# Optimization experiments

Hardware: AMD Instinct MI355X
Metric: run time of the kernel (lower is better)

The kernel has to match this reference:

```python
import jax, jax.numpy as jnp
import numpy as np

S, B, I, O, H, E, K = 128, 32, 512, 512, 512, 8, 2


def setup_inputs() -> dict:
    key = jax.random.key(0)
    ks = jax.random.split(key, 6)
    s = 0.02
    return {
        "x": jax.random.normal(ks[0], (S, B, I), dtype=jnp.float32),
        "router_w": jax.random.normal(ks[1], (I, E), dtype=jnp.float32) * s,
        "router_b": jnp.zeros((E,), dtype=jnp.float32),
        # per-expert LSTM controller params (proxy for DNC_Adapted recurrent expert)
        "Wi": jax.random.normal(ks[2], (E, I, 4 * H), dtype=jnp.float32) * s,
        "Wh": jax.random.normal(ks[3], (E, H, 4 * H), dtype=jnp.float32) * s,
        "b": jnp.zeros((E, 4 * H), dtype=jnp.float32),
        "Wo": jax.random.normal(ks[4], (E, H, O), dtype=jnp.float32) * s,
        "bo": jnp.zeros((E, O), dtype=jnp.float32),
    }


def _expert(x_seq, Wi, Wh, b, Wo, bo):
    # x_seq: [S, B, I] (dense, zero-padded at non-routed positions, as in the
    # original per-expert dispatch); single-layer LSTM controller + output proj.
    Bsz = x_seq.shape[1]
    Hd = Wh.shape[0]

    def step(carry, xt):
        h, c = carry
        gates = xt @ Wi + h @ Wh + b            # [B, 4H]
        i_, f_, g_, o_ = jnp.split(gates, 4, axis=-1)
        c = jax.nn.sigmoid(f_) * c + jax.nn.sigmoid(i_) * jnp.tanh(g_)
        h = jax.nn.sigmoid(o_) * jnp.tanh(c)
        return (h, c), h @ Wo + bo              # [B, O]

    init = (jnp.zeros((Bsz, Hd), x_seq.dtype), jnp.zeros((Bsz, Hd), x_seq.dtype))
    _, ys = jax.lax.scan(step, init, x_seq)
    return ys                                   # [S, B, O]


def reference(x, router_w, router_b, Wi, Wh, b, Wo, bo):
    S_, B_, I_ = x.shape
    N = S_ * B_
    flat_x = x.reshape(N, I_)
    logits = flat_x @ router_w + router_b        # [N, E]
    top_vals, top_idx = jax.lax.top_k(logits, K) # [N, K]
    rw = jax.nn.softmax(top_vals, axis=1)        # routing weights over top-k

    # mask[k, e, n] = 1 if token n routed to expert e at rank k
    mask = (top_idx.T[:, None, :] == jnp.arange(E)[None, :, None]).astype(x.dtype)
    # dense zero-padded per-(k, expert) inputs, matching the original dispatch
    expert_x = (mask[..., None] * flat_x[None, None]).reshape(K, E, S_, B_, I_)

    run_e = jax.vmap(_expert, in_axes=(0, 0, 0, 0, 0, 0))            # over experts
    run_ke = jax.vmap(run_e, in_axes=(0, None, None, None, None, None))  # over k
    out = run_ke(expert_x, Wi, Wh, b, Wo, bo)    # [K, E, S, B, O]
    out = out.reshape(K, E, N, -1)

    # scatter-add weighted expert outputs back to token positions
    y = jnp.einsum('ken,nk,keno->no', mask, rw, out)
    return y.reshape(S_, B_, -1)
```

## Files before the change

### kernel.cpp

```cpp
#include <hip/hip_runtime.h>
#include <hip/hip_bf16.h>
#include <cstdint>
#include <cstddef>

#define DI __device__ __forceinline__

typedef __bf16 bf16_t;
typedef bf16_t bf16x8 __attribute__((ext_vector_type(8)));
typedef float f32x4 __attribute__((ext_vector_type(4)));
typedef unsigned int u32;
typedef unsigned long long u64;

constexpr int S_ = 128, B_ = 32, I_ = 512, H_ = 512, O_ = 512, E_ = 8;
constexpr int Ntok = S_ * B_;
constexpr int G4 = 4 * H_;
constexpr int ROWS = 64;
constexpr int SLOT = E_ * ROWS * H_;

constexpr size_t OFF_CNT  = 0;
constexpr size_t OFF_BAR  = 64;
constexpr size_t OFF_XCDM = 640;
constexpr size_t OFF_XCDG = 1216;
constexpr size_t OFF_MASK = 2048;
constexpr size_t OFF_HALL = 16384;
constexpr size_t SLOT_B   = (size_t)SLOT * 2;
constexpr size_t ZERO_BYTES = OFF_HALL + SLOT_B;
constexpr size_t OFF_TIDX = OFF_HALL + 129ull * SLOT_B;
constexpr size_t OFF_RW   = OFF_TIDX + (size_t)Ntok * 2 * 4;
constexpr size_t OFF_LIST = OFF_RW + (size_t)Ntok * 2 * 4;
constexpr size_t OFF_WHT  = OFF_LIST + (size_t)E_ * Ntok * 4;
constexpr size_t OFF_WIT  = OFF_WHT + (size_t)E_ * G4 * H_ * 2;
constexpr size_t OFF_WOT  = OFF_WIT + (size_t)E_ * G4 * I_ * 2;
constexpr size_t OFF_XP   = OFF_WOT + (size_t)E_ * O_ * H_ * 2;
constexpr size_t WS_NEED  = OFF_XP + (size_t)Ntok * 2 * G4 * 2;

DI float sigf(float v) { return 1.f / (1.f + __expf(-v)); }
DI float tanh_(float v) { float e = __expf(2.f * v); return 1.f - 2.f / (e + 1.f); }

DI bf16x8 pack8(float4 a, float4 b) {
  bf16x8 r;
  r[0] = (bf16_t)a.x; r[1] = (bf16_t)a.y; r[2] = (bf16_t)a.z; r[3] = (bf16_t)a.w;
  r[4] = (bf16_t)b.x; r[5] = (bf16_t)b.y; r[6] = (bf16_t)b.z; r[7] = (bf16_t)b.w;
  return r;
}

__global__ void k_prep(const float* __restrict__ src, bf16_t* __restrict__ dst,
                       int Cdim, int perm) {
  __shared__ float tile[32][33];
  int ct = blockIdx.x, kt = blockIdx.y, e = blockIdx.z;
  const float* se = src + (size_t)e * 512 * Cdim;
  bf16_t* de = dst + (size_t)e * Cdim * 512;
  int c = threadIdx.x & 31, r0 = threadIdx.x >> 5;
  for (int s = 0; s < 4; s++) {
    int rr = r0 + s * 8;
    tile[rr][c] = se[(size_t)(kt * 32 + rr) * Cdim + ct * 32 + c];
  }
  __syncthreads();
  int kk = threadIdx.x & 31, c0 = threadIdx.x >> 5;
  for (int s = 0; s < 4; s++) {
    int cc = c0 + s * 8;
    int cg = ct * 32 + cc;
    int vc = perm ? (((cg & 511) >> 4) * 64 + (cg >> 9) * 16 + (cg & 15)) : cg;
    int kg = kt * 32 + kk;
    de[(size_t)vc * 512 + (kg ^ ((vc & 7) << 3))] = (bf16_t)tile[kk][cc];
  }
}

__global__ void k_router(const float* __restrict__ x, const float* __restrict__ rww,
                         const float* __restrict__ rwb, int* __restrict__ topidx,
                         float* __restrict__ rwgt, int* __restrict__ lists,
                         int* __restrict__ cnt, u64* __restrict__ rowmask) {
  int n = blockIdx.x * 4 + (threadIdx.x >> 6);
  int l = threadIdx.x & 63;
  const float* xr = x + (size_t)n * I_;
  double acc[8] = {0, 0, 0, 0, 0, 0, 0, 0};
  for (int ii = 0; ii < 8; ii++) {
    int i = l * 8 + ii;
    double xv = (double)xr[i];
    const float* wr = rww + i * 8;
#pragma unroll
    for (int e = 0; e < 8; e++) acc[e] += xv * (double)wr[e];
  }
#pragma unroll
  for (int off = 32; off > 0; off >>= 1)
#pragma unroll
    for (int e = 0; e < 8; e++) acc[e] += __shfl_xor(acc[e], off, 64);
  if (l == 0) {
    double lg[8];
    for (int e = 0; e < 8; e++) lg[e] = acc[e] + (double)rwb[e];
    int e0 = 0;
    for (int e = 1; e < 8; e++) if (lg[e] > lg[e0]) e0 = e;
    int e1 = -1;
    for (int e = 0; e < 8; e++) { if (e == e0) continue; if (e1 < 0 || lg[e] > lg[e1]) e1 = e; }
    double ed = exp(lg[e1] - lg[e0]);
    float p0 = (float)(1.0 / (1.0 + ed));
    float p1 = (float)(ed / (1.0 + ed));
    topidx[n * 2] = e0; topidx[n * 2 + 1] = e1;
    rwgt[n * 2] = p0; rwgt[n * 2 + 1] = p1;
    int t = n >> 5, bi = n & 31;
    int p = atomicAdd(&cnt[e0], 1); lists[e0 * Ntok + p] = n * 2;
    p = atomicAdd(&cnt[e1], 1);     lists[e1 * Ntok + p] = n * 2 + 1;
    atomicOr(&rowmask[e0 * 128 + t], 1ull << bi);
    atomicOr(&rowmask[e1 * 128 + t], 1ull << (32 + bi));
  }
}

DI void gemm64(const bf16_t* Als, const bf16_t* Bls, int wv, int l, f32x4* acc) {
  int ar = l & 15, kg = l >> 4;
  int arow = wv * 16 + ar;
  int aswz = (ar & 7) << 3;
#pragma unroll
  for (int ks = 0; ks < 16; ks++) {
    int kb = ks * 32 + kg * 8;
    bf16x8 a = *(const bf16x8*)&Als[arow * 512 + (kb ^ aswz)];
#pragma unroll
    for (int q = 0; q < 4; q++) {
      bf16x8 b = *(const bf16x8*)&Bls[(q * 16 + ar) * 512 + (kb ^ aswz)];
      acc[q] = __builtin_amdgcn_mfma_f32_16x16x32_bf16(a, b, acc[q], 0, 0, 0);
    }
  }
}

__launch_bounds__(256, 1)
__global__ void k_xp(const float* __restrict__ x, const bf16_t* __restrict__ Wit,
                     const int* __restrict__ lists, const int* __restrict__ cnt,
                     bf16_t* __restrict__ xp) {
  __shared__ bf16_t Als[64 * 512];
  __shared__ bf16_t Bls[64 * 512];
  __shared__ int ents[64];
  int e = blockIdx.z, ct = blockIdx.x, rt = blockIdx.y;
  int count = cnt[e];
  int rbase = rt * 64;
  if (rbase >= count) return;
  int tid = threadIdx.x;
  if (tid < 64) ents[tid] = (rbase + tid < count) ? lists[e * Ntok + rbase + tid] : -1;
  __syncthreads();
  int rr = tid >> 2, qq = tid & 3;
  int ent = ents[rr];
  int swzr = (rr & 7) << 3;
  if (ent >= 0) {
    const float* xr = x + (size_t)(ent >> 1) * I_ + qq * 128;
#pragma unroll
    for (int i2 = 0; i2 < 16; i2++) {
      float4 a = *(const float4*)(xr + i2 * 8);
      float4 b = *(const float4*)(xr + i2 * 8 + 4);
      *(bf16x8*)&Als[rr * 512 + ((qq * 128 + i2 * 8) ^ swzr)] = pack8(a, b);
    }
  } else {
    bf16x8 z;
    for (int j = 0; j < 8; j++) z[j] = (bf16_t)0.f;
#pragma unroll
    for (int i2 = 0; i2 < 16; i2++)
      *(bf16x8*)&Als[rr * 512 + ((qq * 128 + i2 * 8) ^ swzr)] = z;
  }
  const bf16_t* bs = Wit + ((size_t)e * G4 + ct * 64) * 512;
#pragma unroll
  for (int i2 = 0; i2 < 16; i2++) {
    int o = (i2 * 256 + tid) * 8;
    *(bf16x8*)&Bls[o] = *(const bf16x8*)&bs[o];
  }
  __syncthreads();
  f32x4 acc[4];
  for (int q = 0; q < 4; q++) { f32x4 z = {0.f, 0.f, 0.f, 0.f}; acc[q] = z; }
  int l = tid & 63, wv = tid >> 6;
  gemm64(Als, Bls, wv, l, acc);
#pragma unroll
  for (int q = 0; q < 4; q++)
#pragma unroll
    for (int r = 0; r < 4; r++) {
      int rr2 = wv * 16 + ((l >> 4) << 2) + r;
      int ent2 = ents[rr2];
      if (ent2 >= 0)
        xp[(size_t)ent2 * G4 + ct * 64 + q * 16 + (l & 15)] = (bf16_t)acc[q][r];
    }
}

DI void gbar(u32* bar_e, int idx, bool fence) {
  if (fence) __threadfence();
  __syncthreads();
  if (threadIdx.x == 0) {
    __hip_atomic_fetch_add(bar_e, 1u, __ATOMIC_RELAXED, __HIP_MEMORY_SCOPE_AGENT);
    u32 target = 32u * (u32)(idx + 1);
    while (__hip_atomic_load(bar_e, __ATOMIC_RELAXED, __HIP_MEMORY_SCOPE_AGENT) < target)
      __builtin_amdgcn_s_sleep(2);
  }
  __syncthreads();
  if (fence) __threadfence();
}

__launch_bounds__(256, 1)
__global__ void k_rec(const bf16_t* __restrict__ Wht, const bf16_t* __restrict__ xp,
                      const float* __restrict__ bgate, bf16_t* __restrict__ hall,
                      const u64* __restrict__ rowmask, u32* __restrict__ bar,
                      u32* __restrict__ xcdm, u32* __restrict__ xcdg) {
  __shared__ bf16_t Bls[64 * 512];
  int bid = blockIdx.x;
  int e = bid & 7, w = bid >> 3;
  int tid = threadIdx.x, l = tid & 63, wv = tid >> 6;
  const bf16_t* bs = Wht + ((size_t)e * G4 + w * 64) * 512;
#pragma unroll
  for (int i2 = 0; i2 < 16; i2++) {
    int o = (i2 * 256 + tid) * 8;
    *(bf16x8*)&Bls[o] = *(const bf16x8*)&bs[o];
  }
  int jl = l & 15, j = w * 16 + jl;
  float bq[4];
#pragma unroll
  for (int q = 0; q < 4; q++) bq[q] = bgate[e * G4 + q * 512 + j];
  int xcd = __builtin_amdgcn_s_getreg(20 | (3 << 11)) & 15;
  if (tid == 0) {
    __hip_atomic_fetch_or(&xcdm[e * 16], 1u << xcd, __ATOMIC_RELAXED, __HIP_MEMORY_SCOPE_AGENT);
    __hip_atomic_fetch_or(xcdg, 1u << xcd, __ATOMIC_RELAXED, __HIP_MEMORY_SCOPE_AGENT);
  }
  u32* mybar = &bar[e * 16];
  gbar(mybar, 0, true);
  u32 me = __hip_atomic_load(&xcdm[e * 16], __ATOMIC_RELAXED, __HIP_MEMORY_SCOPE_AGENT);
  u32 mg = __hip_atomic_load(xcdg, __ATOMIC_RELAXED, __HIP_MEMORY_SCOPE_AGENT);
  bool fast = (__popc(me) == 1) && (__popc(mg) > 1);
  float creg[4] = {0.f, 0.f, 0.f, 0.f};
  int ar = l & 15, kg = l >> 4;
  int arow = wv * 16 + ar;
  int aswz = (ar & 7) << 3;
  for (int t = 0; t < 128; t++) {
    const bf16_t* hc = hall + (size_t)t * SLOT + e * ROWS * 512;
    bf16x8 af[16];
#pragma unroll
    for (int ks = 0; ks < 16; ks++)
      af[ks] = *(const bf16x8*)&hc[arow * 512 + ks * 32 + kg * 8];
    f32x4 acc[4];
    for (int q = 0; q < 4; q++) { f32x4 z = {0.f, 0.f, 0.f, 0.f}; acc[q] = z; }
#pragma unroll
    for (int ks = 0; ks < 16; ks++) {
      int kb = ks * 32 + kg * 8;
#pragma unroll
      for (int q = 0; q < 4; q++) {
        bf16x8 b = *(const bf16x8*)&Bls[(q * 16 + ar) * 512 + (kb ^ aswz)];
        acc[q] = __builtin_amdgcn_mfma_f32_16x16x32_bf16(af[ks], b, acc[q], 0, 0, 0);
      }
    }
    u64 mask = rowmask[e * 128 + t];
    bf16_t* hn = hall + (size_t)(t + 1) * SLOT + e * ROWS * 512;
#pragma unroll
    for (int r = 0; r < 4; r++) {
      int row = wv * 16 + ((l >> 4) << 2) + r;
      float gi = acc[0][r] + bq[0];
      float gf = acc[1][r] + bq[1];
      float gg = acc[2][r] + bq[2];
      float go = acc[3][r] + bq[3];
      if ((mask >> row) & 1ull) {
        int n2 = ((t << 5) + (row & 31)) * 2 + (row >> 5);
        const bf16_t* xr = xp + (size_t)n2 * G4;
        gi += (float)xr[j];        gf += (float)xr[512 + j];
        gg += (float)xr[1024 + j]; go += (float)xr[1536 + j];
      }
      float cn = sigf(gf) * creg[r] + sigf(gi) * tanh_(gg);
      creg[r] = cn;
      float hv = sigf(go) * tanh_(cn);
      hn[row * 512 + j] = (bf16_t)hv;
    }
    if (t < 127) gbar(mybar, t + 1, !fast);
  }
}

__launch_bounds__(256, 1)
__global__ void k_out(const bf16_t* __restrict__ hall, const bf16_t* __restrict__ Wot,
                      const float* __restrict__ bo, const int* __restrict__ lists,
                      const int* __restrict__ cnt, const float* __restrict__ rwgt,
                      float* __restrict__ y) {
  __shared__ bf16_t Als[64 * 512];
  __shared__ bf16_t Bls[64 * 512];
  __shared__ int ents[64];
  __shared__ float rws[64];
  int e = blockIdx.z, ct = blockIdx.x, rt = blockIdx.y;
  int count = cnt[e];
  if (rt * 64 >= count) return;
  int tid = threadIdx.x;
  if (tid < 64) {
    int ent = (rt * 64 + tid < count) ? lists[e * Ntok + rt * 64 + tid] : -1;
    ents[tid] = ent;
    rws[tid] = (ent >= 0) ? rwgt[ent] : 0.f;
  }
  __syncthreads();
  int rr = tid >> 2, qq = tid & 3;
  int ent = ents[rr];
  int swzr = (rr & 7) << 3;
  if (ent >= 0) {
    int n = ent >> 1, kk = ent & 1, t = n >> 5;
    const bf16_t* hr = hall + (size_t)(t + 1) * SLOT +
                       (size_t)(e * ROWS + kk * 32 + (n & 31)) * 512 + qq * 128;
#pragma unroll
    for (int i2 = 0; i2 < 16; i2++) {
      bf16x8 v = *(const bf16x8*)(hr + i2 * 8);
      *(bf16x8*)&Als[rr * 512 + ((qq * 128 + i2 * 8) ^ swzr)] = v;
    }
  } else {
    bf16x8 z;
    for (int jz = 0; jz < 8; jz++) z[jz] = (bf16_t)0.f;
#pragma unroll
    for (int i2 = 0; i2 < 16; i2++)
      *(bf16x8*)&Als[rr * 512 + ((qq * 128 + i2 * 8) ^ swzr)] = z;
  }
  const bf16_t* bsrc = Wot + ((size_t)e * O_ + ct * 64) * 512;
#pragma unroll
  for (int i2 = 0; i2 < 16; i2++) {
    int o = (i2 * 256 + tid) * 8;
    *(bf16x8*)&Bls[o] = *(const bf16x8*)&bsrc[o];
  }
  __syncthreads();
  f32x4 acc[4];
  for (int q = 0; q < 4; q++) { f32x4 z = {0.f, 0.f, 0.f, 0.f}; acc[q] = z; }
  int l = tid & 63, wv = tid >> 6;
  gemm64(Als, Bls, wv, l, acc);
  float boq[4];
#pragma unroll
  for (int q = 0; q < 4; q++) boq[q] = bo[e * O_ + ct * 64 + q * 16 + (l & 15)];
#pragma unroll
  for (int q = 0; q < 4; q++)
#pragma unroll
    for (int r = 0; r < 4; r++) {
      int rr2 = wv * 16 + ((l >> 4) << 2) + r;
      int ent2 = ents[rr2];
      if (ent2 >= 0) {
        float val = (acc[q][r] + boq[q]) * rws[rr2];
        unsafeAtomicAdd(&y[(size_t)(ent2 >> 1) * O_ + ct * 64 + q * 16 + (l & 15)], val);
      }
    }
}

extern "C" void kernel_launch(void* const* d_in, const int* in_sizes, int n_in,
                              void* d_out, int out_size, void* d_ws, size_t ws_size,
                              hipStream_t stream) {
  (void)in_sizes; (void)n_in;
  const float* x   = (const float*)d_in[0];
  const float* rww = (const float*)d_in[1];
  const float* rwb = (const float*)d_in[2];
  const float* Wi  = (const float*)d_in[3];
  const float* Wh  = (const float*)d_in[4];
  const float* bg  = (const float*)d_in[5];
  const float* Wo  = (const float*)d_in[6];
  const float* bo  = (const float*)d_in[7];
  float* y = (float*)d_out;
  char* ws = (char*)d_ws;

  if (ws_size < WS_NEED) {
    hipMemsetAsync(d_out, 0, (size_t)out_size * 4, stream);
    return;
  }

  int* cnt     = (int*)(ws + OFF_CNT);
  u32* bar     = (u32*)(ws + OFF_BAR);
  u32* xcdm    = (u32*)(ws + OFF_XCDM);
  u32* xcdg    = (u32*)(ws + OFF_XCDG);
  u64* rowmask = (u64*)(ws + OFF_MASK);
  bf16_t* hall = (bf16_t*)(ws + OFF_HALL);
  int* topidx  = (int*)(ws + OFF_TIDX);
  float* rwgt  = (float*)(ws + OFF_RW);
  int* lists   = (int*)(ws + OFF_LIST);
  bf16_t* Wht  = (bf16_t*)(ws + OFF_WHT);
  bf16_t* Wit  = (bf16_t*)(ws + OFF_WIT);
  bf16_t* Wot  = (bf16_t*)(ws + OFF_WOT);
  bf16_t* xp   = (bf16_t*)(ws + OFF_XP);

  hipMemsetAsync(ws, 0, ZERO_BYTES, stream);
  hipMemsetAsync(d_out, 0, (size_t)out_size * 4, stream);

  k_prep<<<dim3(G4 / 32, 16, 8), 256, 0, stream>>>(Wi, Wit, G4, 0);
  k_prep<<<dim3(G4 / 32, 16, 8), 256, 0, stream>>>(Wh, Wht, G4, 1);
  k_prep<<<dim3(O_ / 32, 16, 8), 256, 0, stream>>>(Wo, Wot, O_, 0);
  k_router<<<Ntok / 4, 256, 0, stream>>>(x, rww, rwb, topidx, rwgt, lists, cnt, rowmask);
  k_xp<<<dim3(32, 64, 8), 256, 0, stream>>>(x, Wit, lists, cnt, xp);
  k_rec<<<256, 256, 0, stream>>>(Wht, xp, bg, hall, rowmask, bar, xcdm, xcdg);
  k_out<<<dim3(8, 64, 8), 256, 0, stream>>>(hall, Wot, bo, lists, cnt, rwgt, y);
}
```

Baseline: 1.212 ms.

## Replace counter barrier with per-block flag sync, prefetch interleaved xp, persist tiles

The per-expert atomic-counter barrier in the recurrent kernel becomes per-block step flags that each wave polls across all 32 peer blocks with a wave-wide vote. The xp gate pre-activations are stored gate-interleaved so each row needs one 8-byte load, and that load for step t+1 is issued before the step-t MFMA work. The k_xp and k_out grids shrink to 16 row-tiles that loop over row chunks, so each block loads its weight tile into shared memory once. This aims to cut barrier latency and the exposed global loads on the serial recurrence path, at the cost of more polling traffic.

```diff
diff --git a/kernel.cpp b/kernel.cpp
--- a/kernel.cpp
+++ b/kernel.cpp
@@ -18,10 +18,11 @@
 constexpr int SLOT = E_ * ROWS * H_;
 
 constexpr size_t OFF_CNT  = 0;
-constexpr size_t OFF_BAR  = 64;
-constexpr size_t OFF_XCDM = 640;
-constexpr size_t OFF_XCDG = 1216;
+constexpr size_t OFF_XCDM = 64;
+constexpr size_t OFF_XCDG = 704;
+constexpr size_t OFF_DFL  = 1024;
 constexpr size_t OFF_MASK = 2048;
+constexpr size_t OFF_FLG  = 10240;
 constexpr size_t OFF_HALL = 16384;
 constexpr size_t SLOT_B   = (size_t)SLOT * 2;
 constexpr size_t ZERO_BYTES = OFF_HALL + SLOT_B;
@@ -36,6 +37,7 @@
 
 DI float sigf(float v) { return 1.f / (1.f + __expf(-v)); }
 DI float tanh_(float v) { float e = __expf(2.f * v); return 1.f - 2.f / (e + 1.f); }
+DI float bfu(u32 s) { u32 x = (s & 0xffffu) << 16; return __builtin_bit_cast(float, x); }
 
 DI bf16x8 pack8(float4 a, float4 b) {
   bf16x8 r;
@@ -124,75 +126,66 @@
 __launch_bounds__(256, 1)
 __global__ void k_xp(const float* __restrict__ x, const bf16_t* __restrict__ Wit,
                      const int* __restrict__ lists, const int* __restrict__ cnt,
-                     bf16_t* __restrict__ xp) {
+                     bf16_t* __restrict__ xp2) {
   __shared__ bf16_t Als[64 * 512];
   __shared__ bf16_t Bls[64 * 512];
   __shared__ int ents[64];
-  int e = blockIdx.z, ct = blockIdx.x, rt = blockIdx.y;
+  int e = blockIdx.z, ct = blockIdx.x, rt0 = blockIdx.y;
   int count = cnt[e];
-  int rbase = rt * 64;
-  if (rbase >= count) return;
   int tid = threadIdx.x;
-  if (tid < 64) ents[tid] = (rbase + tid < count) ? lists[e * Ntok + rbase + tid] : -1;
-  __syncthreads();
-  int rr = tid >> 2, qq = tid & 3;
-  int ent = ents[rr];
-  int swzr = (rr & 7) << 3;
-  if (ent >= 0) {
-    const float* xr = x + (size_t)(ent >> 1) * I_ + qq * 128;
-#pragma unroll
-    for (int i2 = 0; i2 < 16; i2++) {
-      float4 a = *(const float4*)(xr + i2 * 8);
-      float4 b = *(const float4*)(xr + i2 * 8 + 4);
-      *(bf16x8*)&Als[rr * 512 + ((qq * 128 + i2 * 8) ^ swzr)] = pack8(a, b);
-    }
-  } else {
-    bf16x8 z;
-    for (int j = 0; j < 8; j++) z[j] = (bf16_t)0.f;
-#pragma unroll
-    for (int i2 = 0; i2 < 16; i2++)
-      *(bf16x8*)&Als[rr * 512 + ((qq * 128 + i2 * 8) ^ swzr)] = z;
-  }
   const bf16_t* bs = Wit + ((size_t)e * G4 + ct * 64) * 512;
 #pragma unroll
   for (int i2 = 0; i2 < 16; i2++) {
     int o = (i2 * 256 + tid) * 8;
     *(bf16x8*)&Bls[o] = *(const bf16x8*)&bs[o];
   }
-  __syncthreads();
-  f32x4 acc[4];
-  for (int q = 0; q < 4; q++) { f32x4 z = {0.f, 0.f, 0.f, 0.f}; acc[q] = z; }
   int l = tid & 63, wv = tid >> 6;
-  gemm64(Als, Bls, wv, l, acc);
-#pragma unroll
-  for (int q = 0; q < 4; q++)
-#pragma unroll
-    for (int r = 0; r < 4; r++) {
-      int rr2 = wv * 16 + ((l >> 4) << 2) + r;
-      int ent2 = ents[rr2];
-      if (ent2 >= 0)
-        xp[(size_t)ent2 * G4 + ct * 64 + q * 16 + (l & 15)] = (bf16_t)acc[q][r];
-    }
-}
-
-DI void gbar(u32* bar_e, int idx, bool fence) {
-  if (fence) __threadfence();
-  __syncthreads();
-  if (threadIdx.x == 0) {
-    __hip_atomic_fetch_add(bar_e, 1u, __ATOMIC_RELAXED, __HIP_MEMORY_SCOPE_AGENT);
-    u32 target = 32u * (u32)(idx + 1);
-    while (__hip_atomic_load(bar_e, __ATOMIC_RELAXED, __HIP_MEMORY_SCOPE_AGENT) < target)
-      __builtin_amdgcn_s_sleep(2);
-  }
-  __syncthreads();
-  if (fence) __threadfence();
+  int rr = tid >> 2, qq = tid & 3;
+  int swzr = (rr & 7) << 3;
+  for (int rbase = rt0 * 64; rbase < count; rbase += 16 * 64) {
+    __syncthreads();
+    if (tid < 64) ents[tid] = (rbase + tid < count) ? lists[e * Ntok + rbase + tid] : -1;
+    __syncthreads();
+    int ent = ents[rr];
+    if (ent >= 0) {
+      const float* xr = x + (size_t)(ent >> 1) * I_ + qq * 128;
+#pragma unroll
+      for (int i2 = 0; i2 < 16; i2++) {
+        float4 a = *(const float4*)(xr + i2 * 8);
+        float4 b = *(const float4*)(xr + i2 * 8 + 4);
+        *(bf16x8*)&Als[rr * 512 + ((qq * 128 + i2 * 8) ^ swzr)] = pack8(a, b);
+      }
+    } else {
+      bf16x8 z;
+      for (int jz = 0; jz < 8; jz++) z[jz] = (bf16_t)0.f;
+#pragma unroll
+      for (int i2 = 0; i2 < 16; i2++)
+        *(bf16x8*)&Als[rr * 512 + ((qq * 128 + i2 * 8) ^ swzr)] = z;
+    }
+    __syncthreads();
+    f32x4 acc[4];
+    for (int q = 0; q < 4; q++) { f32x4 z = {0.f, 0.f, 0.f, 0.f}; acc[q] = z; }
+    gemm64(Als, Bls, wv, l, acc);
+#pragma unroll
+    for (int q = 0; q < 4; q++)
+#pragma unroll
+      for (int r = 0; r < 4; r++) {
+        int rr2 = wv * 16 + ((l >> 4) << 2) + r;
+        int ent2 = ents[rr2];
+        if (ent2 >= 0) {
+          int g = ct * 64 + q * 16 + (l & 15);
+          xp2[(size_t)ent2 * G4 + (size_t)(g & 511) * 4 + (g >> 9)] = (bf16_t)acc[q][r];
+        }
+      }
+  }
 }
 
 __launch_bounds__(256, 1)
-__global__ void k_rec(const bf16_t* __restrict__ Wht, const bf16_t* __restrict__ xp,
+__global__ void k_rec(const bf16_t* __restrict__ Wht, const bf16_t* __restrict__ xp2,
                       const float* __restrict__ bgate, bf16_t* __restrict__ hall,
-                      const u64* __restrict__ rowmask, u32* __restrict__ bar,
-                      u32* __restrict__ xcdm, u32* __restrict__ xcdg) {
+                      const u64* __restrict__ rowmask, u32* __restrict__ flags,
+                      u32* __restrict__ dfl, u32* __restrict__ xcdm,
+                      u32* __restrict__ xcdg) {
   __shared__ bf16_t Bls[64 * 512];
   int bid = blockIdx.x;
   int e = bid & 7, w = bid >> 3;
@@ -211,22 +204,59 @@
   if (tid == 0) {
     __hip_atomic_fetch_or(&xcdm[e * 16], 1u << xcd, __ATOMIC_RELAXED, __HIP_MEMORY_SCOPE_AGENT);
     __hip_atomic_fetch_or(xcdg, 1u << xcd, __ATOMIC_RELAXED, __HIP_MEMORY_SCOPE_AGENT);
-  }
-  u32* mybar = &bar[e * 16];
-  gbar(mybar, 0, true);
+    __hip_atomic_store(&dfl[e * 32 + w], 1u, __ATOMIC_RELEASE, __HIP_MEMORY_SCOPE_AGENT);
+  }
+  for (;;) {
+    u32 f = __hip_atomic_load(&dfl[e * 32 + (l & 31)], __ATOMIC_RELAXED, __HIP_MEMORY_SCOPE_AGENT);
+    if (__all((int)(f >= 1u))) break;
+    __builtin_amdgcn_s_sleep(1);
+  }
+  __builtin_amdgcn_sched_barrier(0);
   u32 me = __hip_atomic_load(&xcdm[e * 16], __ATOMIC_RELAXED, __HIP_MEMORY_SCOPE_AGENT);
   u32 mg = __hip_atomic_load(xcdg, __ATOMIC_RELAXED, __HIP_MEMORY_SCOPE_AGENT);
   bool fast = (__popc(me) == 1) && (__popc(mg) > 1);
+  __syncthreads();
+
   float creg[4] = {0.f, 0.f, 0.f, 0.f};
   int ar = l & 15, kg = l >> 4;
   int arow = wv * 16 + ar;
   int aswz = (ar & 7) << 3;
+  int r0 = wv * 16 + (kg << 2);
+  const ushort* xpu = (const ushort*)xp2;
+
+  uint2 xpc[4], xpn[4];
+  {
+    u64 mk = rowmask[e * 128];
+#pragma unroll
+    for (int r = 0; r < 4; r++) {
+      int row = r0 + r;
+      xpc[r].x = 0; xpc[r].y = 0;
+      if ((mk >> row) & 1ull) {
+        int n2 = ((row & 31)) * 2 + (row >> 5);
+        xpc[r] = *(const uint2*)(xpu + ((size_t)n2 * G4 + j * 4));
+      }
+    }
+  }
+
   for (int t = 0; t < 128; t++) {
     const bf16_t* hc = hall + (size_t)t * SLOT + e * ROWS * 512;
     bf16x8 af[16];
 #pragma unroll
     for (int ks = 0; ks < 16; ks++)
       af[ks] = *(const bf16x8*)&hc[arow * 512 + ks * 32 + kg * 8];
+#pragma unroll
+    for (int r = 0; r < 4; r++) { xpn[r].x = 0; xpn[r].y = 0; }
+    if (t < 127) {
+      u64 mk = rowmask[e * 128 + t + 1];
+#pragma unroll
+      for (int r = 0; r < 4; r++) {
+        int row = r0 + r;
+        if ((mk >> row) & 1ull) {
+          int n2 = (((t + 1) << 5) + (row & 31)) * 2 + (row >> 5);
+          xpn[r] = *(const uint2*)(xpu + ((size_t)n2 * G4 + j * 4));
+        }
+      }
+    }
     f32x4 acc[4];
     for (int q = 0; q < 4; q++) { f32x4 z = {0.f, 0.f, 0.f, 0.f}; acc[q] = z; }
 #pragma unroll
@@ -238,27 +268,36 @@
         acc[q] = __builtin_amdgcn_mfma_f32_16x16x32_bf16(af[ks], b, acc[q], 0, 0, 0);
       }
     }
-    u64 mask = rowmask[e * 128 + t];
     bf16_t* hn = hall + (size_t)(t + 1) * SLOT + e * ROWS * 512;
 #pragma unroll
     for (int r = 0; r < 4; r++) {
-      int row = wv * 16 + ((l >> 4) << 2) + r;
-      float gi = acc[0][r] + bq[0];
-      float gf = acc[1][r] + bq[1];
-      float gg = acc[2][r] + bq[2];
-      float go = acc[3][r] + bq[3];
-      if ((mask >> row) & 1ull) {
-        int n2 = ((t << 5) + (row & 31)) * 2 + (row >> 5);
-        const bf16_t* xr = xp + (size_t)n2 * G4;
-        gi += (float)xr[j];        gf += (float)xr[512 + j];
-        gg += (float)xr[1024 + j]; go += (float)xr[1536 + j];
-      }
+      int row = r0 + r;
+      float gi = acc[0][r] + bq[0] + bfu(xpc[r].x);
+      float gf = acc[1][r] + bq[1] + bfu(xpc[r].x >> 16);
+      float gg = acc[2][r] + bq[2] + bfu(xpc[r].y);
+      float go = acc[3][r] + bq[3] + bfu(xpc[r].y >> 16);
       float cn = sigf(gf) * creg[r] + sigf(gi) * tanh_(gg);
       creg[r] = cn;
-      float hv = sigf(go) * tanh_(cn);
-      hn[row * 512 + j] = (bf16_t)hv;
-    }
-    if (t < 127) gbar(mybar, t + 1, !fast);
+      hn[row * 512 + j] = (bf16_t)(sigf(go) * tanh_(cn));
+    }
+#pragma unroll
+    for (int r = 0; r < 4; r++) xpc[r] = xpn[r];
+    if (t < 127) {
+      __syncthreads();
+      if (!fast) __threadfence();
+      if (tid == 0)
+        __hip_atomic_store(&flags[e * 64 + w], (u32)(t + 1), __ATOMIC_RELAXED,
+                           __HIP_MEMORY_SCOPE_AGENT);
+      u32 tgt = (u32)(t + 1);
+      for (;;) {
+        u32 f = __hip_atomic_load(&flags[e * 64 + (l & 31)], __ATOMIC_RELAXED,
+                                  __HIP_MEMORY_SCOPE_AGENT);
+        if (__all((int)(f >= tgt))) break;
+        __builtin_amdgcn_s_sleep(1);
+      }
+      __builtin_amdgcn_sched_barrier(0);
+      if (!fast) __threadfence();
+    }
   }
 }
 
@@ -271,60 +310,62 @@
   __shared__ bf16_t Bls[64 * 512];
   __shared__ int ents[64];
   __shared__ float rws[64];
-  int e = blockIdx.z, ct = blockIdx.x, rt = blockIdx.y;
+  int e = blockIdx.z, ct = blockIdx.x, rt0 = blockIdx.y;
   int count = cnt[e];
-  if (rt * 64 >= count) return;
   int tid = threadIdx.x;
-  if (tid < 64) {
-    int ent = (rt * 64 + tid < count) ? lists[e * Ntok + rt * 64 + tid] : -1;
-    ents[tid] = ent;
-    rws[tid] = (ent >= 0) ? rwgt[ent] : 0.f;
-  }
-  __syncthreads();
-  int rr = tid >> 2, qq = tid & 3;
-  int ent = ents[rr];
-  int swzr = (rr & 7) << 3;
-  if (ent >= 0) {
-    int n = ent >> 1, kk = ent & 1, t = n >> 5;
-    const bf16_t* hr = hall + (size_t)(t + 1) * SLOT +
-                       (size_t)(e * ROWS + kk * 32 + (n & 31)) * 512 + qq * 128;
-#pragma unroll
-    for (int i2 = 0; i2 < 16; i2++) {
-      bf16x8 v = *(const bf16x8*)(hr + i2 * 8);
-      *(bf16x8*)&Als[rr * 512 + ((qq * 128 + i2 * 8) ^ swzr)] = v;
-    }
-  } else {
-    bf16x8 z;
-    for (int jz = 0; jz < 8; jz++) z[jz] = (bf16_t)0.f;
-#pragma unroll
-    for (int i2 = 0; i2 < 16; i2++)
-      *(bf16x8*)&Als[rr * 512 + ((qq * 128 + i2 * 8) ^ swzr)] = z;
-  }
   const bf16_t* bsrc = Wot + ((size_t)e * O_ + ct * 64) * 512;
 #pragma unroll
   for (int i2 = 0; i2 < 16; i2++) {
     int o = (i2 * 256 + tid) * 8;
     *(bf16x8*)&Bls[o] = *(const bf16x8*)&bsrc[o];
   }
-  __syncthreads();
-  f32x4 acc[4];
-  for (int q = 0; q < 4; q++) { f32x4 z = {0.f, 0.f, 0.f, 0.f}; acc[q] = z; }
   int l = tid & 63, wv = tid >> 6;
-  gemm64(Als, Bls, wv, l, acc);
+  int rr = tid >> 2, qq = tid & 3;
+  int swzr = (rr & 7) << 3;
   float boq[4];
 #pragma unroll
   for (int q = 0; q < 4; q++) boq[q] = bo[e * O_ + ct * 64 + q * 16 + (l & 15)];
-#pragma unroll
-  for (int q = 0; q < 4; q++)
-#pragma unroll
-    for (int r = 0; r < 4; r++) {
-      int rr2 = wv * 16 + ((l >> 4) << 2) + r;
-      int ent2 = ents[rr2];
-      if (ent2 >= 0) {
-        float val = (acc[q][r] + boq[q]) * rws[rr2];
-        unsafeAtomicAdd(&y[(size_t)(ent2 >> 1) * O_ + ct * 64 + q * 16 + (l & 15)], val);
-      }
-    }
+  for (int rbase = rt0 * 64; rbase < count; rbase += 16 * 64) {
+    __syncthreads();
+    if (tid < 64) {
+      int ent = (rbase + tid < count) ? lists[e * Ntok + rbase + tid] : -1;
+      ents[tid] = ent;
+      rws[tid] = (ent >= 0) ? rwgt[ent] : 0.f;
+    }
+    __syncthreads();
+    int ent = ents[rr];
+    if (ent >= 0) {
+      int n = ent >> 1, kk = ent & 1, t = n >> 5;
+      const bf16_t* hr = hall + (size_t)(t + 1) * SLOT +
+                         (size_t)(e * ROWS + kk * 32 + (n & 31)) * 512 + qq * 128;
+#pragma unroll
+      for (int i2 = 0; i2 < 16; i2++) {
+        bf16x8 v = *(const bf16x8*)(hr + i2 * 8);
+        *(bf16x8*)&Als[rr * 512 + ((qq * 128 + i2 * 8) ^ swzr)] = v;
+      }
+    } else {
+      bf16x8 z;
+      for (int jz = 0; jz < 8; jz++) z[jz] = (bf16_t)0.f;
+#pragma unroll
+      for (int i2 = 0; i2 < 16; i2++)
+        *(bf16x8*)&Als[rr * 512 + ((qq * 128 + i2 * 8) ^ swzr)] = z;
+    }
+    __syncthreads();
+    f32x4 acc[4];
+    for (int q = 0; q < 4; q++) { f32x4 z = {0.f, 0.f, 0.f, 0.f}; acc[q] = z; }
+    gemm64(Als, Bls, wv, l, acc);
+#pragma unroll
+    for (int q = 0; q < 4; q++)
+#pragma unroll
+      for (int r = 0; r < 4; r++) {
+        int rr2 = wv * 16 + ((l >> 4) << 2) + r;
+        int ent2 = ents[rr2];
+        if (ent2 >= 0) {
+          float val = (acc[q][r] + boq[q]) * rws[rr2];
+          unsafeAtomicAdd(&y[(size_t)(ent2 >> 1) * O_ + ct * 64 + q * 16 + (l & 15)], val);
+        }
+      }
+  }
 }
 
 extern "C" void kernel_launch(void* const* d_in, const int* in_sizes, int n_in,
@@ -348,10 +389,11 @@
   }
 
   int* cnt     = (int*)(ws + OFF_CNT);
-  u32* bar     = (u32*)(ws + OFF_BAR);
   u32* xcdm    = (u32*)(ws + OFF_XCDM);
   u32* xcdg    = (u32*)(ws + OFF_XCDG);
+  u32* dfl     = (u32*)(ws + OFF_DFL);
   u64* rowmask = (u64*)(ws + OFF_MASK);
+  u32* flags   = (u32*)(ws + OFF_FLG);
   bf16_t* hall = (bf16_t*)(ws + OFF_HALL);
   int* topidx  = (int*)(ws + OFF_TIDX);
   float* rwgt  = (float*)(ws + OFF_RW);
@@ -359,7 +401,7 @@
   bf16_t* Wht  = (bf16_t*)(ws + OFF_WHT);
   bf16_t* Wit  = (bf16_t*)(ws + OFF_WIT);
   bf16_t* Wot  = (bf16_t*)(ws + OFF_WOT);
-  bf16_t* xp   = (bf16_t*)(ws + OFF_XP);
+  bf16_t* xp2  = (bf16_t*)(ws + OFF_XP);
 
   hipMemsetAsync(ws, 0, ZERO_BYTES, stream);
   hipMemsetAsync(d_out, 0, (size_t)out_size * 4, stream);
@@ -368,7 +410,7 @@
   k_prep<<<dim3(G4 / 32, 16, 8), 256, 0, stream>>>(Wh, Wht, G4, 1);
   k_prep<<<dim3(O_ / 32, 16, 8), 256, 0, stream>>>(Wo, Wot, O_, 0);
   k_router<<<Ntok / 4, 256, 0, stream>>>(x, rww, rwb, topidx, rwgt, lists, cnt, rowmask);
-  k_xp<<<dim3(32, 64, 8), 256, 0, stream>>>(x, Wit, lists, cnt, xp);
-  k_rec<<<256, 256, 0, stream>>>(Wht, xp, bg, hall, rowmask, bar, xcdm, xcdg);
-  k_out<<<dim3(8, 64, 8), 256, 0, stream>>>(hall, Wot, bo, lists, cnt, rwgt, y);
-}
+  k_xp<<<dim3(32, 16, 8), 256, 0, stream>>>(x, Wit, lists, cnt, xp2);
+  k_rec<<<256, 256, 0, stream>>>(Wht, xp2, bg, hall, rowmask, flags, dfl, xcdm, xcdg);
+  k_out<<<dim3(8, 16, 8), 256, 0, stream>>>(hall, Wot, bo, lists, cnt, rwgt, y);
+}
```

Result: faster. 987.2 us (-18.6%).
